# Kernel tuning notes

Hardware: AMD Instinct MI355X
Metric: run time of the kernel (lower is better)

The kernel has to match this reference:

```python
import jax, jax.numpy as jnp
import numpy as np

N = 50000   # nodes
E = 800000  # edges
G = 64      # graphs
NEG_SLOPE = 0.2  # PyG GATConv leaky_relu slope


def gat_conv(x, edge_index, edge_attr, W, att_src, att_dst, We, att_edge, bias, num_nodes):
    # PyG GATConv, add_self_loops=False, concat=True, eval (no dropout)
    H, C = att_src.shape
    h = (x @ W).reshape(-1, H, C)                      # [N,H,C]
    a_src = (h * att_src).sum(-1)                      # [N,H]
    a_dst = (h * att_dst).sum(-1)                      # [N,H]
    src, dst = edge_index[0], edge_index[1]
    e = (edge_attr @ We).reshape(-1, H, C)             # [E,H,C]
    a_edge = (e * att_edge).sum(-1)                    # [E,H]
    alpha = a_src[src] + a_dst[dst] + a_edge           # [E,H]
    alpha = jax.nn.leaky_relu(alpha, NEG_SLOPE)
    # segment softmax over incoming edges of each dst node
    amax = jax.ops.segment_max(alpha, dst, num_segments=num_nodes)
    amax = jnp.where(jnp.isfinite(amax), amax, 0.0)
    ex = jnp.exp(alpha - amax[dst])
    denom = jax.ops.segment_sum(ex, dst, num_segments=num_nodes)
    att = ex / (denom[dst] + 1e-16)                    # [E,H]
    msg = h[src] * att[..., None]                      # [E,H,C]
    out = jax.ops.segment_sum(msg, dst, num_segments=num_nodes)
    return out.reshape(num_nodes, H * C) + bias


def setup_inputs() -> dict:
    key = jax.random.key(0)
    ks = jax.random.split(key, 20)
    s = 0.1
    inp = {
        "x": jax.random.normal(ks[0], (N, 128), jnp.float32),
        "edge_index": jax.random.randint(ks[1], (2, E), 0, N, dtype=jnp.int32),
        "edge_attr": jax.random.normal(ks[2], (E, 1), jnp.float32),
        "batch": jnp.sort(jax.random.randint(ks[3], (N,), 0, G, dtype=jnp.int32)),
        # layer 1: 128 -> 4 heads x 32
        "W1": jax.random.normal(ks[4], (128, 128), jnp.float32) * s,
        "as1": jax.random.normal(ks[5], (4, 32), jnp.float32) * s,
        "ad1": jax.random.normal(ks[6], (4, 32), jnp.float32) * s,
        "We1": jax.random.normal(ks[7], (1, 128), jnp.float32) * s,
        "ae1": jax.random.normal(ks[8], (4, 32), jnp.float32) * s,
        "b1": jnp.zeros((128,), jnp.float32),
        # layer 2: 128 -> 1 head x 64
        "W2": jax.random.normal(ks[9], (128, 64), jnp.float32) * s,
        "as2": jax.random.normal(ks[10], (1, 64), jnp.float32) * s,
        "ad2": jax.random.normal(ks[11], (1, 64), jnp.float32) * s,
        "We2": jax.random.normal(ks[12], (1, 64), jnp.float32) * s,
        "ae2": jax.random.normal(ks[13], (1, 64), jnp.float32) * s,
        "b2": jnp.zeros((64,), jnp.float32),
        # prediction head
        "Wp": jax.random.normal(ks[14], (64, 1), jnp.float32) * s,
        "bp": jnp.zeros((1,), jnp.float32),
    }
    return inp


def reference(x, edge_index, edge_attr, batch, W1, as1, ad1, We1, ae1, b1,
              W2, as2, ad2, We2, ae2, b2, Wp, bp):
    h = gat_conv(x, edge_index, edge_attr, W1, as1, ad1, We1, ae1, b1, N)
    h = jax.nn.relu(h)  # dropout p=0.0, eval mode
    h = gat_conv(h, edge_index, edge_attr, W2, as2, ad2, We2, ae2, b2, N)
    # per-graph mean pooling (vectorized replacement of the python loop)
    counts = jax.ops.segment_sum(jnp.ones((N,), h.dtype), batch, num_segments=G)
    sums = jax.ops.segment_sum(h, batch, num_segments=G)   # [G,64]
    mean = sums / counts[:, None]
    out = mean @ Wp + bp                                   # [G,1]
    return out.squeeze(-1)                                 # [G]
```

## Files before the change

### kernel.cpp

```cpp
#include <hip/hip_runtime.h>
#include <hip/hip_bf16.h>

typedef unsigned short u16;
typedef unsigned int u32;

#define MAXB 2048
#define POOL_MAXG 64

typedef __attribute__((ext_vector_type(8))) short bf16x8;
typedef __attribute__((ext_vector_type(4))) float f32x4;

__device__ __forceinline__ float bf2f(u16 u) { return __uint_as_float(((u32)u) << 16); }
__device__ __forceinline__ float bl(u32 u) { return __uint_as_float(u << 16); }
__device__ __forceinline__ float bh(u32 u) { return __uint_as_float(u & 0xffff0000u); }
__device__ __forceinline__ u16 f2bf(float f) {
    u32 u = __float_as_uint(f);
    u += 0x7fffu + ((u >> 16) & 1u);
    return (u16)(u >> 16);
}
__device__ __forceinline__ float lrelu(float x) { return x > 0.f ? x : 0.2f * x; }
__device__ __forceinline__ int clampi(int v, int lo, int hi) {
    return v < lo ? lo : (v > hi ? hi : v);
}
__device__ __forceinline__ float load1(const void* base, int idx, int f32) {
    return f32 ? ((const float*)base)[idx] : bf2f(((const u16*)base)[idx]);
}
__device__ __forceinline__ float cexpf(float a) {
    return __builtin_amdgcn_exp2f(fminf(a, 30.f) * 1.4426950408889634f);
}

__global__ void k_init(const u32* __restrict__ xw, int* __restrict__ flag,
                       int* __restrict__ bcnt, int B,
                       const void* We1, const void* ae1, const void* We2, const void* ae2,
                       const void* as1, const void* ad1, const void* as2, const void* ad2,
                       float* __restrict__ consts, float* __restrict__ pool, int psize) {
    __shared__ int sf;
    int t = threadIdx.x;
    for (int i = t; i < B; i += 256) bcnt[i] = 0;
    if (t < 64) {
        int cnt = 0;
        #pragma unroll
        for (int j = 0; j < 4; j++) {
            u32 w = xw[t * 4 + j];
            int e0 = (int)((w >> 7) & 0xffu);
            int e1 = (int)((w >> 23) & 0xffu);
            cnt += (e0 >= 0x60 && e0 <= 0x8f);
            cnt += (e1 >= 0x60 && e1 <= 0x8f);
        }
        #pragma unroll
        for (int off = 32; off > 0; off >>= 1) cnt += __shfl_xor(cnt, off);
        if (t == 0) { int v = (cnt < 480) ? 1 : 0; *flag = v; sf = v; }
    }
    __syncthreads();
    int f = sf;
    for (int i = t; i < psize; i += 256) pool[i] = 0.f;
    if (t < 4) {
        float s = 0.f;
        for (int c = 0; c < 32; c++) s += load1(We1, t * 32 + c, f) * load1(ae1, t * 32 + c, f);
        consts[t] = s;
    } else if (t == 4) {
        float s = 0.f;
        for (int c = 0; c < 64; c++) s += load1(We2, c, f) * load1(ae2, c, f);
        consts[4] = s;
    }
    if (t < 128) {
        consts[8 + t] = load1(as1, t, f);
        consts[136 + t] = load1(ad1, t, f);
    }
    if (t < 64) {
        consts[264 + t] = load1(as2, t, f);
        consts[328 + t] = load1(ad2, t, f);
    }
}

template <int NC>
__global__ __launch_bounds__(256, 2) void k_gemm_mfma(
    const void* __restrict__ X, const void* __restrict__ Wg,
    const int* __restrict__ flag, int fXovr, u16* __restrict__ Y,
    const float* __restrict__ consts, float* __restrict__ casrc,
    float* __restrict__ cadst, int nrows) {
    constexpr int NCT = NC / 16;
    __shared__ __align__(16) u16 Bf[2][NCT][4][64][8];

    const int f = *flag;
    const bool fX = (fXovr < 0) ? (f != 0) : (fXovr != 0);
    const bool fW = (f != 0);
    const int tid = threadIdx.x;
    const int wid = tid >> 6, lane = tid & 63;

    for (int idx = tid; idx < NCT * 4 * 64; idx += 256) {
        int l = idx & 63;
        int s = (idx >> 6) & 3;
        int t = idx >> 8;
        int col = t * 16 + (l & 15);
        int k0 = s * 32 + (l >> 4) * 8;
        u16 hi[8], lo[8];
        #pragma unroll
        for (int j = 0; j < 8; j++) {
            int k = k0 + j;
            int srow = (NC == 64) ? ((k & 1) * 64 + (k >> 1)) : k;
            float v = fW ? ((const float*)Wg)[srow * NC + col]
                         : bf2f(((const u16*)Wg)[srow * NC + col]);
            u16 h = f2bf(v);
            hi[j] = h;
            lo[j] = fW ? f2bf(v - bf2f(h)) : (u16)0;
        }
        uint4 hv, lv;
        hv.x = (u32)hi[0] | ((u32)hi[1] << 16);
        hv.y = (u32)hi[2] | ((u32)hi[3] << 16);
        hv.z = (u32)hi[4] | ((u32)hi[5] << 16);
        hv.w = (u32)hi[6] | ((u32)hi[7] << 16);
        lv.x = (u32)lo[0] | ((u32)lo[1] << 16);
        lv.y = (u32)lo[2] | ((u32)lo[3] << 16);
        lv.z = (u32)lo[4] | ((u32)lo[5] << 16);
        lv.w = (u32)lo[6] | ((u32)lo[7] << 16);
        *(uint4*)&Bf[0][t][s][l][0] = hv;
        *(uint4*)&Bf[1][t][s][l][0] = lv;
    }
    __syncthreads();

    const int tiles = (nrows + 63) >> 6;
    for (int tile = blockIdx.x; tile < tiles; tile += gridDim.x) {
        const int rowbase = tile * 64 + wid * 16;
        const int arow = rowbase + (lane & 15);
        const bool rv = arow < nrows;

        bf16x8 ahi[4], alo[4];
        #pragma unroll
        for (int s = 0; s < 4; s++) {
            int koff = s * 32 + (lane >> 4) * 8;
            u16 h[8], l8[8];
            #pragma unroll
            for (int j = 0; j < 8; j++) { h[j] = 0; l8[j] = 0; }
            if (rv) {
                if (fX) {
                    const float* xp = (const float*)X + (size_t)arow * 128 + koff;
                    float4 a = *(const float4*)xp;
                    float4 b = *(const float4*)(xp + 4);
                    float vv[8];
                    vv[0] = a.x; vv[1] = a.y; vv[2] = a.z; vv[3] = a.w;
                    vv[4] = b.x; vv[5] = b.y; vv[6] = b.z; vv[7] = b.w;
                    #pragma unroll
                    for (int j = 0; j < 8; j++) {
                        h[j] = f2bf(vv[j]);
                        l8[j] = f2bf(vv[j] - bf2f(h[j]));
                    }
                } else {
                    const u16* xp = (const u16*)X + (size_t)arow * 128 + koff;
                    uint4 q = *(const uint4*)xp;
                    h[0] = (u16)q.x; h[1] = (u16)(q.x >> 16);
                    h[2] = (u16)q.y; h[3] = (u16)(q.y >> 16);
                    h[4] = (u16)q.z; h[5] = (u16)(q.z >> 16);
                    h[6] = (u16)q.w; h[7] = (u16)(q.w >> 16);
                }
            }
            bf16x8 vh, vl;
            #pragma unroll
            for (int j = 0; j < 8; j++) { vh[j] = (short)h[j]; vl[j] = (short)l8[j]; }
            ahi[s] = vh; alo[s] = vl;
        }

        f32x4 acc[NCT];
        #pragma unroll
        for (int t = 0; t < NCT; t++) acc[t] = (f32x4){0.f, 0.f, 0.f, 0.f};
        #pragma unroll
        for (int s = 0; s < 4; s++) {
            #pragma unroll
            for (int t = 0; t < NCT; t++) {
                bf16x8 bhi = *(const bf16x8*)&Bf[0][t][s][lane][0];
                acc[t] = __builtin_amdgcn_mfma_f32_16x16x32_bf16(ahi[s], bhi, acc[t], 0, 0, 0);
                if (fW) {
                    bf16x8 blo = *(const bf16x8*)&Bf[1][t][s][lane][0];
                    acc[t] = __builtin_amdgcn_mfma_f32_16x16x32_bf16(ahi[s], blo, acc[t], 0, 0, 0);
                }
                if (fX) {
                    acc[t] = __builtin_amdgcn_mfma_f32_16x16x32_bf16(alo[s], bhi, acc[t], 0, 0, 0);
                }
            }
        }

        #pragma unroll
        for (int reg = 0; reg < 4; reg++) {
            int r = rowbase + (lane >> 4) * 4 + reg;
            if (r < nrows) {
                if constexpr (NC == 128) {
                    #pragma unroll
                    for (int t = 0; t < 4; t++) {
                        u32 w = (u32)f2bf(acc[t][reg]) | ((u32)f2bf(acc[t + 4][reg]) << 16);
                        ((u32*)Y)[(size_t)r * 64 + t * 16 + (lane & 15)] = w;
                    }
                } else {
                    #pragma unroll
                    for (int t = 0; t < 4; t++)
                        Y[(size_t)r * 64 + t * 16 + (lane & 15)] = f2bf(acc[t][reg]);
                }
            }
        }

        if (casrc) {
            const int l16 = lane & 15;
            if constexpr (NC == 128) {
                #pragma unroll
                for (int reg = 0; reg < 4; reg++) {
                    int r = rowbase + (lane >> 4) * 4 + reg;
                    float pA[4] = {0.f, 0.f, 0.f, 0.f};
                    float pD[4] = {0.f, 0.f, 0.f, 0.f};
                    #pragma unroll
                    for (int t = 0; t < 4; t++) {
                        int p = t * 16 + l16;
                        int g = t >> 1;
                        pA[g]     += acc[t][reg]     * consts[8 + p];
                        pD[g]     += acc[t][reg]     * consts[136 + p];
                        pA[g + 2] += acc[t + 4][reg] * consts[72 + p];
                        pD[g + 2] += acc[t + 4][reg] * consts[200 + p];
                    }
                    #pragma unroll
                    for (int off = 1; off < 16; off <<= 1) {
                        #pragma unroll
                        for (int g = 0; g < 4; g++) {
                            pA[g] += __shfl_xor(pA[g], off);
                            pD[g] += __shfl_xor(pD[g], off);
                        }
                    }
                    if (l16 == 0 && r < nrows) {
                        #pragma unroll
                        for (int g = 0; g < 4; g++) {
                            casrc[r * 4 + g] = pA[g];
                            cadst[r * 4 + g] = pD[g];
                        }
                    }
                }
            } else {
                #pragma unroll
                for (int reg = 0; reg < 4; reg++) {
                    int r = rowbase + (lane >> 4) * 4 + reg;
                    float s1 = 0.f, s2 = 0.f;
                    #pragma unroll
                    for (int t = 0; t < 4; t++) {
                        int p = t * 16 + l16;
                        s1 += acc[t][reg] * consts[264 + p];
                        s2 += acc[t][reg] * consts[328 + p];
                    }
                    #pragma unroll
                    for (int off = 1; off < 16; off <<= 1) {
                        s1 += __shfl_xor(s1, off);
                        s2 += __shfl_xor(s2, off);
                    }
                    if (l16 == 0 && r < nrows) { casrc[r] = s1; cadst[r] = s2; }
                }
            }
        }
    }
}

__global__ __launch_bounds__(256) void k_bhist2(const int* __restrict__ dst,
                                                int* __restrict__ bcnt, int E, int n, int B) {
    __shared__ int lh[MAXB];
    for (int i = threadIdx.x; i < B; i += 256) lh[i] = 0;
    __syncthreads();
    int stride = gridDim.x * 256;
    for (int e = blockIdx.x * 256 + threadIdx.x; e < E; e += stride) {
        int d = clampi(dst[e], 0, n - 1);
        atomicAdd(&lh[d >> 8], 1);
    }
    __syncthreads();
    for (int i = threadIdx.x; i < B; i += 256)
        if (lh[i]) atomicAdd(&bcnt[i], lh[i]);
}
__global__ void k_bscan(const int* __restrict__ bcnt, int* __restrict__ bbase,
                        int* __restrict__ bfront, int* __restrict__ roff,
                        int B, int N, int E) {
    __shared__ int buf[256];
    __shared__ int carry;
    int t = threadIdx.x;
    if (t == 0) carry = 0;
    __syncthreads();
    for (int base = 0; base < B; base += 256) {
        int k = base + t;
        int v = (k < B) ? bcnt[k] : 0;
        buf[t] = v;
        __syncthreads();
        for (int off = 1; off < 256; off <<= 1) {
            int u = (t >= off) ? buf[t - off] : 0;
            __syncthreads();
            buf[t] += u;
            __syncthreads();
        }
        int excl = carry + buf[t] - v;
        if (k < B) { bbase[k] = excl; bfront[k] = excl; }
        __syncthreads();
        if (t == 0) carry += buf[255];
        __syncthreads();
    }
    if (t == 0) { bbase[B] = carry; roff[N] = E; }
}
__global__ void k_zero(int* __restrict__ p, int n) {
    int i = blockIdx.x * 256 + threadIdx.x;
    if (i < n) p[i] = 0;
}
__global__ __launch_bounds__(256) void k_bhist(const int* __restrict__ dst,
                                               int* __restrict__ cnt, int* __restrict__ bcnt,
                                               int E, int n, int B) {
    __shared__ int lh[MAXB];
    for (int i = threadIdx.x; i < B; i += 256) lh[i] = 0;
    __syncthreads();
    int stride = gridDim.x * 256;
    for (int e = blockIdx.x * 256 + threadIdx.x; e < E; e += stride) {
        int d = clampi(dst[e], 0, n - 1);
        atomicAdd(&cnt[d], 1);
        atomicAdd(&lh[d >> 8], 1);
    }
    __syncthreads();
    for (int i = threadIdx.x; i < B; i += 256)
        if (lh[i]) atomicAdd(&bcnt[i], lh[i]);
}
__global__ void k_scan1(const int* __restrict__ cnt, int* __restrict__ part,
                        int* __restrict__ bsum, int n) {
    __shared__ int buf[256];
    int i = blockIdx.x * 256 + threadIdx.x;
    int v = (i < n) ? cnt[i] : 0;
    buf[threadIdx.x] = v;
    __syncthreads();
    for (int off = 1; off < 256; off <<= 1) {
        int t = (threadIdx.x >= off) ? buf[threadIdx.x - off] : 0;
        __syncthreads();
        buf[threadIdx.x] += t;
        __syncthreads();
    }
    if (i < n) part[i] = buf[threadIdx.x];
    if (threadIdx.x == 255) bsum[blockIdx.x] = buf[255];
}
__global__ void k_scan3b(int* __restrict__ roff, const int* __restrict__ bsum,
                         int* __restrict__ rpos, int n, int nb) {
    __shared__ int buf[256];
    int t = threadIdx.x;
    int v = (t < nb) ? bsum[t] : 0;
    buf[t] = v;
    __syncthreads();
    for (int off = 1; off < 256; off <<= 1) {
        int u = (t >= off) ? buf[t - off] : 0;
        __syncthreads();
        buf[t] += u;
        __syncthreads();
    }
    __shared__ int excl[256];
    excl[t] = buf[t] - v;
    __syncthreads();
    int i = blockIdx.x * 256 + t;
    if (i > n) return;
    int val;
    if (i == 0) { val = 0; roff[0] = 0; }
    else { val = roff[i] + excl[(i - 1) >> 8]; roff[i] = val; }
    if (i < n) rpos[i] = val;
}
__global__ __launch_bounds__(256) void k_binA(
    const int* __restrict__ dst, const int* __restrict__ src, const void* eattr,
    const int* __restrict__ flag, int* __restrict__ bfront, int2* __restrict__ stagedA,
    int E, int n, int B) {
    __shared__ int lhist[MAXB];
    __shared__ int lbase[MAXB];
    int f = *flag;
    constexpr int T = 2048;
    for (int tile = blockIdx.x; (long long)tile * T < E; tile += gridDim.x) {
        int base = tile * T;
        for (int i = threadIdx.x; i < B; i += 256) lhist[i] = 0;
        __syncthreads();
        int sj0, sj1, sj2, sj3, sj4, sj5, sj6, sj7;
        int dj0, dj1, dj2, dj3, dj4, dj5, dj6, dj7;
        int rj0, rj1, rj2, rj3, rj4, rj5, rj6, rj7;
        int ej0, ej1, ej2, ej3, ej4, ej5, ej6, ej7;
        #define BINA_LOAD(J, SJ, DJ, RJ, EJ)                                   \
        {                                                                      \
            int idx = base + (J) * 256 + threadIdx.x;                          \
            bool v = idx < E;                                                  \
            int d = v ? clampi(dst[idx], 0, n - 1) : 0;                        \
            SJ = v ? clampi(src[idx], 0, n - 1) : 0;                           \
            EJ = v ? __float_as_int(load1(eattr, idx, f)) : 0;                 \
            DJ = d;                                                            \
            RJ = v ? atomicAdd(&lhist[d >> 8], 1) : -1;                        \
        }
        BINA_LOAD(0, sj0, dj0, rj0, ej0)
        BINA_LOAD(1, sj1, dj1, rj1, ej1)
        BINA_LOAD(2, sj2, dj2, rj2, ej2)
        BINA_LOAD(3, sj3, dj3, rj3, ej3)
        BINA_LOAD(4, sj4, dj4, rj4, ej4)
        BINA_LOAD(5, sj5, dj5, rj5, ej5)
        BINA_LOAD(6, sj6, dj6, rj6, ej6)
        BINA_LOAD(7, sj7, dj7, rj7, ej7)
        #undef BINA_LOAD
        __syncthreads();
        for (int i = threadIdx.x; i < B; i += 256) {
            int c = lhist[i];
            lbase[i] = c ? atomicAdd(&bfront[i], c) : 0;
        }
        __syncthreads();
        #define BINA_STORE(SJ, DJ, RJ, EJ)                                     \
        if (RJ >= 0) {                                                         \
            long long q = (long long)lbase[DJ >> 8] + RJ;                      \
            if (q >= 0 && q < E) {                                             \
                int2 v2;                                                       \
                v2.x = (SJ & 0xFFFFFF) | ((DJ & 255) << 24);                   \
                v2.y = EJ;                                                     \
                stagedA[q] = v2;                                               \
            }                                                                  \
        }
        BINA_STORE(sj0, dj0, rj0, ej0)
        BINA_STORE(sj1, dj1, rj1, ej1)
        BINA_STORE(sj2, dj2, rj2, ej2)
        BINA_STORE(sj3, dj3, rj3, ej3)
        BINA_STORE(sj4, dj4, rj4, ej4)
        BINA_STORE(sj5, dj5, rj5, ej5)
        BINA_STORE(sj6, dj6, rj6, ej6)
        BINA_STORE(sj7, dj7, rj7, ej7)
        #undef BINA_STORE
        __syncthreads();
    }
}
__global__ __launch_bounds__(256) void k_binB2(
    const int2* __restrict__ stagedA, const int* __restrict__ bbase,
    int* __restrict__ roff, int2* __restrict__ edata, int N, int E, int B) {
    __shared__ int lcnt[256];
    __shared__ int buf[256];
    __shared__ int lpos[256];
    int k = blockIdx.x;
    int t = threadIdx.x;
    lcnt[t] = 0;
    __syncthreads();
    int lo = clampi(bbase[k], 0, E);
    int hi = clampi(bbase[k + 1], lo, E);
    for (int i = lo + t; i < hi; i += 256)
        atomicAdd(&lcnt[(stagedA[i].x >> 24) & 255], 1);
    __syncthreads();
    int v = lcnt[t];
    buf[t] = v;
    __syncthreads();
    for (int off = 1; off < 256; off <<= 1) {
        int u = (t >= off) ? buf[t - off] : 0;
        __syncthreads();
        buf[t] += u;
        __syncthreads();
    }
    int pos = lo + buf[t] - v;
    int dn = (k << 8) + t;
    if (dn < N) roff[dn] = pos;
    lpos[t] = pos;
    __syncthreads();
    for (int i = lo + t; i < hi; i += 256) {
        int2 a = stagedA[i];
        int p = atomicAdd(&lpos[(a.x >> 24) & 255], 1);
        if (p >= 0 && p < E) edata[p] = make_int2(a.x & 0xFFFFFF, a.y);
    }
}
__global__ void k_scatter(const int* __restrict__ dst, const int* __restrict__ src,
                          const void* eattr, const int* __restrict__ flag,
                          int* __restrict__ rpos, int2* __restrict__ edata, int E, int n) {
    int f = *flag;
    int e = blockIdx.x * 256 + threadIdx.x;
    if (e < E) {
        int d = clampi(dst[e], 0, n - 1);
        int s = clampi(src[e], 0, n - 1);
        float ea = load1(eattr, e, f);
        int p = atomicAdd(&rpos[d], 1);
        if (p >= 0 && p < E) {
            int2 v; v.x = s; v.y = __float_as_int(ea);
            edata[p] = v;
        }
    }
}

__global__ __launch_bounds__(256) void k_gat1c(
    const u32* __restrict__ hp, const float* __restrict__ asrc, const float* __restrict__ adst,
    const int2* __restrict__ edata, const int* __restrict__ roff,
    const int* __restrict__ flag, const float* __restrict__ consts, const void* bias,
    u32* __restrict__ out, int n, int E) {
    __shared__ float4 wls[4][64];
    int f = *flag;
    int gtid = blockIdx.x * 256 + threadIdx.x;
    int wv = gtid >> 6, lane = gtid & 63;
    int wid = (threadIdx.x >> 6);
    int nw = (gridDim.x * 256) >> 6;
    const float c0 = consts[0], c1 = consts[1], c2 = consts[2], c3 = consts[3];
    const int hl = lane & 31;
    const int sel = lane >> 5;
    const int p0 = hl * 2;
    const int phsel = hl >> 4;
    const float biasA0 = load1(bias, p0, f);
    const float biasB0 = load1(bias, 64 + p0, f);
    const float biasA1 = load1(bias, p0 + 1, f);
    const float biasB1 = load1(bias, 64 + p0 + 1, f);
    const int ghsel = lane >> 5;
    const float gbiasA = load1(bias, lane, f);
    const float gbiasB = load1(bias, 64 + lane, f);

    for (int db = wv * 2; db < n; db += nw * 2) {
        int d = db + sel;
        bool dv = d < n;
        int dcl = dv ? d : 0;
        int s0 = dv ? clampi(roff[d], 0, E) : 0;
        int s1 = dv ? clampi(roff[d + 1], s0, E) : 0;
        int deg = s1 - s0;

        if (__all(deg <= 32)) {
            float4 adv = *(const float4*)&adst[(size_t)dcl * 4];
            bool v = hl < deg;
            int s = 0;
            float e0 = 0.f, e1 = 0.f, e2 = 0.f, e3 = 0.f;
            if (v) {
                int2 ed = edata[s0 + hl];
                s = ed.x;
                float ea = __int_as_float(ed.y);
                float4 av = *(const float4*)&asrc[(size_t)s * 4];
                e0 = cexpf(lrelu(av.x + adv.x + ea * c0));
                e1 = cexpf(lrelu(av.y + adv.y + ea * c1));
                e2 = cexpf(lrelu(av.z + adv.z + ea * c2));
                e3 = cexpf(lrelu(av.w + adv.w + ea * c3));
            }
            float d0 = e0, d1 = e1, d2 = e2, d3 = e3;
            #pragma unroll
            for (int off = 16; off > 0; off >>= 1) {
                d0 += __shfl_xor(d0, off); d1 += __shfl_xor(d1, off);
                d2 += __shfl_xor(d2, off); d3 += __shfl_xor(d3, off);
            }
            float i0 = 1.f / (d0 + 1e-16f), i1 = 1.f / (d1 + 1e-16f);
            float i2 = 1.f / (d2 + 1e-16f), i3 = 1.f / (d3 + 1e-16f);
            wls[wid][lane] = make_float4(e0 * i0, e1 * i1, e2 * i2, e3 * i3);

            int degm = max(deg, __shfl_xor(deg, 32));
            int base = sel * 32;
            float aA0 = 0.f, aB0 = 0.f, aA1 = 0.f, aB1 = 0.f;
            for (int j = 0; j < degm; j += 4) {
                int j0 = base + j, j1 = base + j + 1, j2 = base + j + 2, j3 = base + j + 3;
                int sa = __shfl(s, j0), sb = __shfl(s, j1);
                int sc_ = __shfl(s, j2), sd = __shfl(s, j3);
                float4 wa = wls[wid][j0], wb = wls[wid][j1];
                float4 wc = wls[wid][j2], wd = wls[wid][j3];
                uint2 ha = *(const uint2*)(hp + (size_t)sa * 64 + p0);
                uint2 hb = *(const uint2*)(hp + (size_t)sb * 64 + p0);
                uint2 hc = *(const uint2*)(hp + (size_t)sc_ * 64 + p0);
                uint2 hd = *(const uint2*)(hp + (size_t)sd * 64 + p0);
                float wAa = phsel ? wa.y : wa.x, wBa = phsel ? wa.w : wa.z;
                float wAb = phsel ? wb.y : wb.x, wBb = phsel ? wb.w : wb.z;
                float wAc = phsel ? wc.y : wc.x, wBc = phsel ? wc.w : wc.z;
                float wAd = phsel ? wd.y : wd.x, wBd = phsel ? wd.w : wd.z;
                aA0 += wAa * bl(ha.x); aB0 += wBa * bh(ha.x);
                aA1 += wAa * bl(ha.y); aB1 += wBa * bh(ha.y);
                aA0 += wAb * bl(hb.x); aB0 += wBb * bh(hb.x);
                aA1 += wAb * bl(hb.y); aB1 += wBb * bh(hb.y);
                aA0 += wAc * bl(hc.x); aB0 += wBc * bh(hc.x);
                aA1 += wAc * bl(hc.y); aB1 += wBc * bh(hc.y);
                aA0 += wAd * bl(hd.x); aB0 += wBd * bh(hd.x);
                aA1 += wAd * bl(hd.y); aB1 += wBd * bh(hd.y);
            }
            if (dv) {
                u32 w0 = (u32)f2bf(fmaxf(aA0 + biasA0, 0.f))
                       | ((u32)f2bf(fmaxf(aB0 + biasB0, 0.f)) << 16);
                u32 w1 = (u32)f2bf(fmaxf(aA1 + biasA1, 0.f))
                       | ((u32)f2bf(fmaxf(aB1 + biasB1, 0.f)) << 16);
                *(uint2*)(out + (size_t)d * 64 + p0) = make_uint2(w0, w1);
            }
        } else {
            for (int q = 0; q < 2; q++) {
                int dq = db + q;
                if (dq >= n) break;
                int t0 = clampi(roff[dq], 0, E);
                int t1 = clampi(roff[dq + 1], t0, E);
                int dg = t1 - t0;
                float4 adv = *(const float4*)&adst[(size_t)dq * 4];
                if (dg <= 64) {
                    bool v = lane < dg;
                    int s = 0;
                    float e0 = 0.f, e1 = 0.f, e2 = 0.f, e3 = 0.f;
                    if (v) {
                        int2 ed = edata[t0 + lane];
                        s = ed.x;
                        float ea = __int_as_float(ed.y);
                        float4 av = *(const float4*)&asrc[(size_t)s * 4];
                        e0 = cexpf(lrelu(av.x + adv.x + ea * c0));
                        e1 = cexpf(lrelu(av.y + adv.y + ea * c1));
                        e2 = cexpf(lrelu(av.z + adv.z + ea * c2));
                        e3 = cexpf(lrelu(av.w + adv.w + ea * c3));
                    }
                    float d0 = e0, d1 = e1, d2 = e2, d3 = e3;
                    #pragma unroll
                    for (int off = 32; off > 0; off >>= 1) {
                        d0 += __shfl_xor(d0, off); d1 += __shfl_xor(d1, off);
                        d2 += __shfl_xor(d2, off); d3 += __shfl_xor(d3, off);
                    }
                    float i0 = 1.f / (d0 + 1e-16f), i1 = 1.f / (d1 + 1e-16f);
                    float i2 = 1.f / (d2 + 1e-16f), i3 = 1.f / (d3 + 1e-16f);
                    wls[wid][lane] = make_float4(e0 * i0, e1 * i1, e2 * i2, e3 * i3);

                    float aA0 = 0.f, aB0 = 0.f, aA1 = 0.f, aB1 = 0.f;
                    for (int j = 0; j < dg; j += 4) {
                        int j0 = j + sel, j1 = j + 2 + sel;
                        int sa = __shfl(s, j0), sb = __shfl(s, j1);
                        float4 wa = wls[wid][j0], wb = wls[wid][j1];
                        uint2 ha = *(const uint2*)(hp + (size_t)sa * 64 + p0);
                        uint2 hb = *(const uint2*)(hp + (size_t)sb * 64 + p0);
                        float wAa = phsel ? wa.y : wa.x, wBa = phsel ? wa.w : wa.z;
                        float wAb = phsel ? wb.y : wb.x, wBb = phsel ? wb.w : wb.z;
                        aA0 += wAa * bl(ha.x); aB0 += wBa * bh(ha.x);
                        aA1 += wAa * bl(ha.y); aB1 += wBa * bh(ha.y);
                        aA0 += wAb * bl(hb.x); aB0 += wBb * bh(hb.x);
                        aA1 += wAb * bl(hb.y); aB1 += wBb * bh(hb.y);
                    }
                    aA0 += __shfl_xor(aA0, 32); aB0 += __shfl_xor(aB0, 32);
                    aA1 += __shfl_xor(aA1, 32); aB1 += __shfl_xor(aB1, 32);
                    if (lane < 32) {
                        u32 w0 = (u32)f2bf(fmaxf(aA0 + biasA0, 0.f))
                               | ((u32)f2bf(fmaxf(aB0 + biasB0, 0.f)) << 16);
                        u32 w1 = (u32)f2bf(fmaxf(aA1 + biasA1, 0.f))
                               | ((u32)f2bf(fmaxf(aB1 + biasB1, 0.f)) << 16);
                        *(uint2*)(out + (size_t)dq * 64 + p0) = make_uint2(w0, w1);
                    }
                } else {
                    float d0 = 0.f, d1 = 0.f, d2 = 0.f, d3 = 0.f;
                    for (int idx = t0 + lane; idx < t1; idx += 64) {
                        int2 ed = edata[idx];
                        float ea = __int_as_float(ed.y);
                        float4 av = *(const float4*)&asrc[(size_t)ed.x * 4];
                        d0 += cexpf(lrelu(av.x + adv.x + ea * c0));
                        d1 += cexpf(lrelu(av.y + adv.y + ea * c1));
                        d2 += cexpf(lrelu(av.z + adv.z + ea * c2));
                        d3 += cexpf(lrelu(av.w + adv.w + ea * c3));
                    }
                    #pragma unroll
                    for (int off = 32; off > 0; off >>= 1) {
                        d0 += __shfl_xor(d0, off); d1 += __shfl_xor(d1, off);
                        d2 += __shfl_xor(d2, off); d3 += __shfl_xor(d3, off);
                    }
                    float i0 = 1.f / (d0 + 1e-16f), i1 = 1.f / (d1 + 1e-16f);
                    float i2 = 1.f / (d2 + 1e-16f), i3 = 1.f / (d3 + 1e-16f);
                    float iA = ghsel ? i1 : i0, iB = ghsel ? i3 : i2;
                    float cA = ghsel ? c1 : c0, cB = ghsel ? c3 : c2;
                    float aA = ghsel ? adv.y : adv.x, aB = ghsel ? adv.w : adv.z;
                    float accA = 0.f, accB = 0.f;
                    for (int idx = t0; idx < t1; idx++) {
                        int2 ed = edata[idx];
                        float ea = __int_as_float(ed.y);
                        float4 av = *(const float4*)&asrc[(size_t)ed.x * 4];
                        float wA = cexpf(lrelu((ghsel ? av.y : av.x) + aA + ea * cA)) * iA;
                        float wB = cexpf(lrelu((ghsel ? av.w : av.z) + aB + ea * cB)) * iB;
                        u32 hw = hp[(size_t)ed.x * 64 + lane];
                        accA += wA * bl(hw);
                        accB += wB * bh(hw);
                    }
                    float rA = fmaxf(accA + gbiasA, 0.f);
                    float rB = fmaxf(accB + gbiasB, 0.f);
                    out[(size_t)dq * 64 + lane] = (u32)f2bf(rA) | ((u32)f2bf(rB) << 16);
                }
            }
        }
    }
}

__global__ __launch_bounds__(256) void k_gat2c(
    const u16* __restrict__ h, const float* __restrict__ asrc, const float* __restrict__ adst,
    const int2* __restrict__ edata, const int* __restrict__ roff,
    const int* __restrict__ flag, const float* __restrict__ consts, const void* bias,
    u16* __restrict__ out, int n, int E) {
    __shared__ float wls[4][64];
    int f = *flag;
    int gtid = blockIdx.x * 256 + threadIdx.x;
    int wv = gtid >> 6, lane = gtid & 63;
    int wid = (threadIdx.x >> 6);
    int nw = (gridDim.x * 256) >> 6;
    const float C = consts[4];
    const int hl = lane & 31;
    const int sel = lane >> 5;
    const int p0 = hl * 2;
    const float bias0 = load1(bias, p0, f);
    const float bias1 = load1(bias, p0 + 1, f);
    const float gbias = load1(bias, lane, f);

    for (int db = wv * 2; db < n; db += nw * 2) {
        int d = db + sel;
        bool dv = d < n;
        int s0 = dv ? clampi(roff[d], 0, E) : 0;
        int s1 = dv ? clampi(roff[d + 1], s0, E) : 0;
        int deg = s1 - s0;
        float ad = dv ? adst[d] : 0.f;

        if (__all(deg <= 32)) {
            bool v = hl < deg;
            int s = 0;
            float e = 0.f;
            if (v) {
                int2 ed = edata[s0 + hl];
                s = ed.x;
                e = cexpf(lrelu(asrc[s] + ad + __int_as_float(ed.y) * C));
            }
            float den = e;
            #pragma unroll
            for (int off = 16; off > 0; off >>= 1) den += __shfl_xor(den, off);
            float inv = 1.f / (den + 1e-16f);
            wls[wid][lane] = e * inv;

            int degm = max(deg, __shfl_xor(deg, 32));
            int base = sel * 32;
            float a0 = 0.f, a1 = 0.f;
            for (int j = 0; j < degm; j += 4) {
                int j0 = base + j, j1 = base + j + 1, j2 = base + j + 2, j3 = base + j + 3;
                int sa = __shfl(s, j0), sb = __shfl(s, j1);
                int sc_ = __shfl(s, j2), sd = __shfl(s, j3);
                float wa = wls[wid][j0], wb = wls[wid][j1];
                float wc = wls[wid][j2], wd = wls[wid][j3];
                u32 ha = *(const u32*)(h + (size_t)sa * 64 + p0);
                u32 hb = *(const u32*)(h + (size_t)sb * 64 + p0);
                u32 hc = *(const u32*)(h + (size_t)sc_ * 64 + p0);
                u32 hd = *(const u32*)(h + (size_t)sd * 64 + p0);
                a0 += wa * bl(ha) + wb * bl(hb) + wc * bl(hc) + wd * bl(hd);
                a1 += wa * bh(ha) + wb * bh(hb) + wc * bh(hc) + wd * bh(hd);
            }
            if (dv) {
                u32 w = (u32)f2bf(a0 + bias0) | ((u32)f2bf(a1 + bias1) << 16);
                *(u32*)(out + (size_t)d * 64 + p0) = w;
            }
        } else {
            for (int q = 0; q < 2; q++) {
                int dq = db + q;
                if (dq >= n) break;
                int t0 = clampi(roff[dq], 0, E);
                int t1 = clampi(roff[dq + 1], t0, E);
                int dg = t1 - t0;
                float adq = adst[dq];
                if (dg <= 64) {
                    bool v = lane < dg;
                    int s = 0;
                    float e = 0.f;
                    if (v) {
                        int2 ed = edata[t0 + lane];
                        s = ed.x;
                        e = cexpf(lrelu(asrc[s] + adq + __int_as_float(ed.y) * C));
                    }
                    float den = e;
                    #pragma unroll
                    for (int off = 32; off > 0; off >>= 1) den += __shfl_xor(den, off);
                    float inv = 1.f / (den + 1e-16f);
                    wls[wid][lane] = e * inv;

                    float a0 = 0.f, a1 = 0.f;
                    for (int j = 0; j < dg; j += 4) {
                        int j0 = j + sel, j1 = j + 2 + sel;
                        int sa = __shfl(s, j0), sb = __shfl(s, j1);
                        float wa = wls[wid][j0], wb = wls[wid][j1];
                        u32 ha = *(const u32*)(h + (size_t)sa * 64 + p0);
                        u32 hb = *(const u32*)(h + (size_t)sb * 64 + p0);
                        a0 += wa * bl(ha) + wb * bl(hb);
                        a1 += wa * bh(ha) + wb * bh(hb);
                    }
                    a0 += __shfl_xor(a0, 32);
                    a1 += __shfl_xor(a1, 32);
                    if (lane < 32) {
                        u32 w = (u32)f2bf(a0 + bias0) | ((u32)f2bf(a1 + bias1) << 16);
                        *(u32*)(out + (size_t)dq * 64 + p0) = w;
                    }
                } else {
                    float den = 0.f;
                    for (int idx = t0 + lane; idx < t1; idx += 64) {
                        int2 ed = edata[idx];
                        den += cexpf(lrelu(asrc[ed.x] + adq + __int_as_float(ed.y) * C));
                    }
                    #pragma unroll
                    for (int off = 32; off > 0; off >>= 1) den += __shfl_xor(den, off);
                    float inv = 1.f / (den + 1e-16f);
                    float acc = 0.f;
                    for (int idx = t0; idx < t1; idx++) {
                        int2 ed = edata[idx];
                        float w = cexpf(lrelu(asrc[ed.x] + adq
                                              + __int_as_float(ed.y) * C)) * inv;
                        acc += w * bf2f(h[(size_t)ed.x * 64 + lane]);
                    }
                    out[(size_t)dq * 64 + lane] = f2bf(acc + gbias);
                }
            }
        }
    }
}

__global__ __launch_bounds__(256) void k_gat1f(
    const u32* __restrict__ hp, const float* __restrict__ asrc, const float* __restrict__ adst,
    const int2* __restrict__ edata, const int* __restrict__ roff,
    const int* __restrict__ flag, const float* __restrict__ consts, const void* bias,
    u32* __restrict__ out, int n, int E) {
    int f = *flag;
    int gtid = blockIdx.x * 256 + threadIdx.x;
    int wv = gtid >> 6, lane = gtid & 63;
    int nw = (gridDim.x * 256) >> 6;
    const float c0 = consts[0], c1 = consts[1], c2 = consts[2], c3 = consts[3];
    const int hsel = lane >> 5;
    const float biasA = load1(bias, lane, f);
    const float biasB = load1(bias, 64 + lane, f);

    for (int d = wv; d < n; d += nw) {
        int s0 = clampi(roff[d], 0, E);
        int s1 = clampi(roff[d + 1], s0, E);
        float4 adv = *(const float4*)&adst[d * 4];
        float d0 = 0.f, d1 = 0.f, d2 = 0.f, d3 = 0.f;
        for (int idx = s0 + lane; idx < s1; idx += 64) {
            int2 ed = edata[idx];
            float ea = __int_as_float(ed.y);
            float4 av = *(const float4*)&asrc[(size_t)ed.x * 4];
            d0 += cexpf(lrelu(av.x + adv.x + ea * c0));
            d1 += cexpf(lrelu(av.y + adv.y + ea * c1));
            d2 += cexpf(lrelu(av.z + adv.z + ea * c2));
            d3 += cexpf(lrelu(av.w + adv.w + ea * c3));
        }
        #pragma unroll
        for (int off = 32; off > 0; off >>= 1) {
            d0 += __shfl_xor(d0, off); d1 += __shfl_xor(d1, off);
            d2 += __shfl_xor(d2, off); d3 += __shfl_xor(d3, off);
        }
        float i0 = 1.f / (d0 + 1e-16f), i1 = 1.f / (d1 + 1e-16f);
        float i2 = 1.f / (d2 + 1e-16f), i3 = 1.f / (d3 + 1e-16f);
        float iA = hsel ? i1 : i0, iB = hsel ? i3 : i2;
        float cA = hsel ? c1 : c0, cB = hsel ? c3 : c2;
        float aA = hsel ? adv.y : adv.x, aB = hsel ? adv.w : adv.z;

        float accA = 0.f, accB = 0.f;
        for (int idx = s0; idx < s1; idx++) {
            int2 ed = edata[idx];
            float ea = __int_as_float(ed.y);
            float4 av = *(const float4*)&asrc[(size_t)ed.x * 4];
            float wA = cexpf(lrelu((hsel ? av.y : av.x) + aA + ea * cA)) * iA;
            float wB = cexpf(lrelu((hsel ? av.w : av.z) + aB + ea * cB)) * iB;
            u32 hw = hp[(size_t)ed.x * 64 + lane];
            accA += wA * bl(hw);
            accB += wB * bh(hw);
        }
        float rA = fmaxf(accA + biasA, 0.f);
        float rB = fmaxf(accB + biasB, 0.f);
        out[(size_t)d * 64 + lane] = (u32)f2bf(rA) | ((u32)f2bf(rB) << 16);
    }
}

__global__ __launch_bounds__(256) void k_gat2f(
    const u16* __restrict__ h, const float* __restrict__ asrc, const float* __restrict__ adst,
    const int2* __restrict__ edata, const int* __restrict__ roff,
    const int* __restrict__ flag, const float* __restrict__ consts, const void* bias,
    u16* __restrict__ out, int n, int E) {
    int f = *flag;
    int gtid = blockIdx.x * 256 + threadIdx.x;
    int wv = gtid >> 6, lane = gtid & 63;
    int nw = (gridDim.x * 256) >> 6;
    const float C = consts[4];
    const float biasL = load1(bias, lane, f);

    for (int d = wv; d < n; d += nw) {
        int s0 = clampi(roff[d], 0, E);
        int s1 = clampi(roff[d + 1], s0, E);
        float ad = adst[d];
        float den = 0.f;
        for (int idx = s0 + lane; idx < s1; idx += 64) {
            int2 ed = edata[idx];
            den += cexpf(lrelu(asrc[ed.x] + ad + __int_as_float(ed.y) * C));
        }
        #pragma unroll
        for (int off = 32; off > 0; off >>= 1) den += __shfl_xor(den, off);
        float inv = 1.f / (den + 1e-16f);

        float acc = 0.f;
        for (int idx = s0; idx < s1; idx++) {
            int2 ed = edata[idx];
            float w = cexpf(lrelu(asrc[ed.x] + ad + __int_as_float(ed.y) * C)) * inv;
            acc += w * bf2f(h[(size_t)ed.x * 64 + lane]);
        }
        out[(size_t)d * 64 + lane] = f2bf(acc + biasL);
    }
}

__global__ __launch_bounds__(256) void k_pool2(
    const u16* __restrict__ agg2, const int* __restrict__ batch,
    float* __restrict__ pool, float* __restrict__ cnt, int n, int G, int rpb) {
    __shared__ float lp[POOL_MAXG * 64];
    __shared__ float lc[POOL_MAXG];
    int t = threadIdx.x;
    for (int i = t; i < G * 64; i += 256) lp[i] = 0.f;
    for (int i = t; i < G; i += 256) lc[i] = 0.f;
    __syncthreads();
    int lane = t & 63;
    int rl = t >> 6;
    int r0 = blockIdx.x * rpb;
    int r1 = min(r0 + rpb, n);
    float acc = 0.f, cacc = 0.f;
    int curg = -1;
    for (int j = r0 + rl; j < r1; j += 4) {
        int g = clampi(batch[j], 0, G - 1);
        float v = bf2f(agg2[(size_t)j * 64 + lane]);
        if (g != curg) {
            if (curg >= 0) {
                atomicAdd(&lp[curg * 64 + lane], acc);
                if (lane == 0) atomicAdd(&lc[curg], cacc);
            }
            acc = 0.f; cacc = 0.f; curg = g;
        }
        acc += v; cacc += 1.f;
    }
    if (curg >= 0) {
        atomicAdd(&lp[curg * 64 + lane], acc);
        if (lane == 0) atomicAdd(&lc[curg], cacc);
    }
    __syncthreads();
    for (int i = t; i < G * 64; i += 256) {
        float v = lp[i];
        if (v != 0.f) atomicAdd(&pool[i], v);
    }
    for (int i = t; i < G; i += 256) {
        float v = lc[i];
        if (v != 0.f) atomicAdd(&cnt[i], v);
    }
}

__global__ void k_pool(const u16* __restrict__ agg2, const int* __restrict__ batch,
                       float* __restrict__ pool, float* __restrict__ cnt, int n, int G) {
    int t = blockIdx.x * 256 + threadIdx.x;
    int nb8 = (n + 7) / 8;
    if (t >= nb8 * 64) return;
    int base = (t >> 6) * 8;
    int c = t & 63;
    int end = min(base + 8, n);
    float acc = 0.f, cacc = 0.f;
    int curg = clampi(batch[base], 0, G - 1);
    for (int j = base; j < end; j++) {
        int g = clampi(batch[j], 0, G - 1);
        if (g != curg) {
            atomicAdd(&pool[curg * 64 + c], acc);
            if (c == 0) atomicAdd(&cnt[curg], cacc);
            acc = 0.f; cacc = 0.f; curg = g;
        }
        acc += bf2f(agg2[(size_t)j * 64 + c]);
        cacc += 1.f;
    }
    atomicAdd(&pool[curg * 64 + c], acc);
    if (c == 0) atomicAdd(&cnt[curg], cacc);
}

__global__ void k_head(const float* __restrict__ pool, const float* __restrict__ cnt,
                       const void* Wp, const void* bp, const int* __restrict__ flag,
                       void* out, int G) {
    int f = *flag;
    int g = threadIdx.x;
    if (g >= G) return;
    float s = 0.f;
    for (int c = 0; c < 64; c++) s += pool[g * 64 + c] * load1(Wp, c, f);
    float cv = cnt[g];
    if (!(cv > 0.f)) cv = 1.f;
    float r = s / cv + load1(bp, 0, f);
    if (f) ((float*)out)[g] = r;
    else   ((u16*)out)[g] = f2bf(r);
}

extern "C" void kernel_launch(void* const* d_in, const int* in_sizes, int n_in,
                              void* d_out, int out_size, void* d_ws, size_t ws_size,
                              hipStream_t stream) {
    const void* x    = d_in[0];
    const int* ei    = (const int*)d_in[1];
    const void* eattr = d_in[2];
    const int* batch = (const int*)d_in[3];
    const void* W1   = d_in[4];
    const void* as1  = d_in[5];
    const void* ad1  = d_in[6];
    const void* We1  = d_in[7];
    const void* ae1  = d_in[8];
    const void* b1   = d_in[9];
    const void* W2   = d_in[10];
    const void* as2  = d_in[11];
    const void* ad2  = d_in[12];
    const void* We2  = d_in[13];
    const void* ae2  = d_in[14];
    const void* b2   = d_in[15];
    const void* Wp   = d_in[16];
    const void* bp   = d_in[17];

    const int N = in_sizes[3];
    const int E = in_sizes[2];
    const int G = out_size;
    const int* src = ei;
    const int* dst = ei + E;
    const int B = (N + 255) >> 8;

    char* p = (char*)d_ws;
    auto alloc = [&](size_t bytes) -> char* {
        char* r = p;
        p += (bytes + 255) & ~(size_t)255;
        return r;
    };
    int* flag    = (int*)alloc(32);
    float* consts = (float*)alloc(2048);
    int* roff    = (int*)alloc((size_t)(N + 1) * 4);
    int* rpos    = (int*)alloc((size_t)N * 4);
    int* bsum    = (int*)alloc(256 * 4);
    int* bcnt    = (int*)alloc((size_t)(MAXB * 3 + 1) * 4);
    int* bbase   = bcnt + MAXB;
    int* bfront  = bbase + MAXB + 1;
    int2* edata  = (int2*)alloc((size_t)E * 8);
    float* pool  = (float*)alloc((size_t)(G * 64 + G) * 4);
    float* cnt   = pool + (size_t)G * 64;
    float* asrc1 = (float*)alloc((size_t)N * 4 * 4);
    float* adst1 = (float*)alloc((size_t)N * 4 * 4);
    float* asrc2 = asrc1;
    float* adst2 = adst1;
    u16* agg1    = (u16*)alloc((size_t)N * 128 * 2);
    u16* h1      = (u16*)alloc((size_t)N * 128 * 2);
    u16* h2      = h1;
    u16* agg2    = h1 + (size_t)N * 64;
    int2* stagedA = (int2*)alloc((size_t)E * 8);
    size_t full_need = (size_t)(p - (char*)d_ws);
    const bool cached = (ws_size >= full_need);
    const bool binned = cached && (B <= MAXB) && (N <= (1 << 24));

    const int GG = (N + 127) >> 7;

    k_init<<<1, 256, 0, stream>>>((const u32*)x, flag, bcnt, B,
                                  We1, ae1, We2, ae2, as1, ad1, as2, ad2,
                                  consts, pool, G * 64 + G);
    k_gemm_mfma<128><<<GG, 256, 0, stream>>>(x, W1, flag, -1, h1, consts,
                                             asrc1, adst1, N);

    if (binned) {
        k_bhist2<<<512, 256, 0, stream>>>(dst, bcnt, E, N, B);
        k_bscan<<<1, 256, 0, stream>>>(bcnt, bbase, bfront, roff, B, N, E);
        k_binA<<<(E + 2047) / 2048, 256, 0, stream>>>(dst, src, eattr, flag, bfront,
                                                      stagedA, E, N, B);
        k_binB2<<<B, 256, 0, stream>>>(stagedA, bbase, roff, edata, N, E, B);
    } else {
        int NB = (N + 255) / 256;
        k_zero<<<(N + 255) / 256, 256, 0, stream>>>(rpos, N);
        k_bhist<<<512, 256, 0, stream>>>(dst, rpos, bcnt, E, N, B);
        k_scan1<<<NB, 256, 0, stream>>>(rpos, roff + 1, bsum, N);
        k_scan3b<<<(N + 256) / 256, 256, 0, stream>>>(roff, bsum, rpos, N, NB);
        k_scatter<<<(E + 255) / 256, 256, 0, stream>>>(dst, src, eattr, flag, rpos,
                                                       edata, E, N);
    }

    int gatBlocks = (N * 64 + 255) / 256;
    if (cached) {
        k_gat1c<<<gatBlocks, 256, 0, stream>>>((const u32*)h1, asrc1, adst1, edata, roff,
                                               flag, consts, b1, (u32*)agg1, N, E);
    } else {
        k_gat1f<<<gatBlocks, 256, 0, stream>>>((const u32*)h1, asrc1, adst1, edata, roff,
                                               flag, consts, b1, (u32*)agg1, N, E);
    }
    k_gemm_mfma<64><<<GG, 256, 0, stream>>>(agg1, W2, flag, 0, h2, consts,
                                            asrc2, adst2, N);
    if (cached) {
        k_gat2c<<<gatBlocks, 256, 0, stream>>>(h2, asrc2, adst2, edata, roff, flag,
                                               consts, b2, agg2, N, E);
    } else {
        k_gat2f<<<gatBlocks, 256, 0, stream>>>(h2, asrc2, adst2, edata, roff, flag,
                                               consts, b2, agg2, N, E);
    }
    if (G <= POOL_MAXG) {
        int rpb = (N + 1023) / 1024;
        if (rpb < 8) rpb = 8;
        int pblocks = (N + rpb - 1) / rpb;
        k_pool2<<<pblocks, 256, 0, stream>>>(agg2, batch, pool, cnt, N, G, rpb);
    } else {
        k_pool<<<(((N + 7) / 8) * 64 + 255) / 256, 256, 0, stream>>>(agg2, batch, pool,
                                                                     cnt, N, G);
    }
    k_head<<<1, 64, 0, stream>>>(pool, cnt, Wp, bp, flag, d_out, G);
}
```

Before: 283.5 us.

## Coalesce weight staging and process two row tiles per block in MFMA GEMM

Weight staging into shared memory now reads W with contiguous float4/uint4 loads and scatters the elements into the MFMA fragment layout, replacing strided scalar global reads. The grid-stride tile loop is replaced by a fixed two-tile-per-block scheme. Both tiles' A fragments are loaded up front and the MFMAs are interleaved, so each B fragment read from LDS is reused twice and there is more independent MFMA work in flight. This doubles accumulator and A-register usage, which may reduce occupancy. It also relies on the launch grid covering all tiles in two passes, otherwise rows would go unprocessed.

```diff
diff --git a/kernel.cpp b/kernel.cpp
--- a/kernel.cpp
+++ b/kernel.cpp
@@ -88,44 +88,60 @@
     const int tid = threadIdx.x;
     const int wid = tid >> 6, lane = tid & 63;
 
-    for (int idx = tid; idx < NCT * 4 * 64; idx += 256) {
-        int l = idx & 63;
-        int s = (idx >> 6) & 3;
-        int t = idx >> 8;
-        int col = t * 16 + (l & 15);
-        int k0 = s * 32 + (l >> 4) * 8;
-        u16 hi[8], lo[8];
-        #pragma unroll
-        for (int j = 0; j < 8; j++) {
-            int k = k0 + j;
-            int srow = (NC == 64) ? ((k & 1) * 64 + (k >> 1)) : k;
-            float v = fW ? ((const float*)Wg)[srow * NC + col]
-                         : bf2f(((const u16*)Wg)[srow * NC + col]);
-            u16 h = f2bf(v);
-            hi[j] = h;
-            lo[j] = fW ? f2bf(v - bf2f(h)) : (u16)0;
-        }
-        uint4 hv, lv;
-        hv.x = (u32)hi[0] | ((u32)hi[1] << 16);
-        hv.y = (u32)hi[2] | ((u32)hi[3] << 16);
-        hv.z = (u32)hi[4] | ((u32)hi[5] << 16);
-        hv.w = (u32)hi[6] | ((u32)hi[7] << 16);
-        lv.x = (u32)lo[0] | ((u32)lo[1] << 16);
-        lv.y = (u32)lo[2] | ((u32)lo[3] << 16);
-        lv.z = (u32)lo[4] | ((u32)lo[5] << 16);
-        lv.w = (u32)lo[6] | ((u32)lo[7] << 16);
-        *(uint4*)&Bf[0][t][s][l][0] = hv;
-        *(uint4*)&Bf[1][t][s][l][0] = lv;
-    }
-    __syncthreads();
-
-    const int tiles = (nrows + 63) >> 6;
-    for (int tile = blockIdx.x; tile < tiles; tile += gridDim.x) {
-        const int rowbase = tile * 64 + wid * 16;
+    if (fW) {
+        const float* W4 = (const float*)Wg;
+        for (int g = tid; g < 128 * NC / 4; g += 256) {
+            int e = g * 4;
+            int r = e / NC;
+            int c = e % NC;
+            int k = (NC == 64) ? ((r < 64) ? 2 * r : 2 * (r - 64) + 1) : r;
+            int s = k >> 5;
+            int kk = k & 31;
+            int lhi = (kk >> 3) << 4;
+            int j = kk & 7;
+            float4 v = *(const float4*)(W4 + e);
+            float vv[4] = {v.x, v.y, v.z, v.w};
+            #pragma unroll
+            for (int q = 0; q < 4; q++) {
+                int col = c + q;
+                int t = col >> 4, l = lhi | (col & 15);
+                u16 h = f2bf(vv[q]);
+                Bf[0][t][s][l][j] = h;
+                Bf[1][t][s][l][j] = f2bf(vv[q] - bf2f(h));
+            }
+        }
+    } else {
+        const u16* Wb = (const u16*)Wg;
+        for (int g = tid; g < 128 * NC / 8; g += 256) {
+            int e = g * 8;
+            int r = e / NC;
+            int c = e % NC;
+            int k = (NC == 64) ? ((r < 64) ? 2 * r : 2 * (r - 64) + 1) : r;
+            int s = k >> 5;
+            int kk = k & 31;
+            int lhi = (kk >> 3) << 4;
+            int j = kk & 7;
+            uint4 v = *(const uint4*)(Wb + e);
+            u16 arr[8] = {(u16)v.x, (u16)(v.x >> 16), (u16)v.y, (u16)(v.y >> 16),
+                          (u16)v.z, (u16)(v.z >> 16), (u16)v.w, (u16)(v.w >> 16)};
+            #pragma unroll
+            for (int q = 0; q < 8; q++) {
+                int col = c + q;
+                int t = col >> 4, l = lhi | (col & 15);
+                Bf[0][t][s][l][j] = arr[q];
+            }
+        }
+    }
+    __syncthreads();
+
+    const int tileIds[2] = {(int)blockIdx.x, (int)(blockIdx.x + gridDim.x)};
+
+    bf16x8 ahi[2][4], alo[2][4];
+    #pragma unroll
+    for (int tt = 0; tt < 2; tt++) {
+        const int rowbase = tileIds[tt] * 64 + wid * 16;
         const int arow = rowbase + (lane & 15);
         const bool rv = arow < nrows;
-
-        bf16x8 ahi[4], alo[4];
         #pragma unroll
         for (int s = 0; s < 4; s++) {
             int koff = s * 32 + (lane >> 4) * 8;
@@ -157,28 +173,38 @@
             bf16x8 vh, vl;
             #pragma unroll
             for (int j = 0; j < 8; j++) { vh[j] = (short)h[j]; vl[j] = (short)l8[j]; }
-            ahi[s] = vh; alo[s] = vl;
-        }
-
-        f32x4 acc[NCT];
+            ahi[tt][s] = vh; alo[tt][s] = vl;
+        }
+    }
+
+    f32x4 acc[2][NCT];
+    #pragma unroll
+    for (int tt = 0; tt < 2; tt++)
         #pragma unroll
-        for (int t = 0; t < NCT; t++) acc[t] = (f32x4){0.f, 0.f, 0.f, 0.f};
+        for (int t = 0; t < NCT; t++) acc[tt][t] = (f32x4){0.f, 0.f, 0.f, 0.f};
+    #pragma unroll
+    for (int s = 0; s < 4; s++) {
         #pragma unroll
-        for (int s = 0; s < 4; s++) {
-            #pragma unroll
-            for (int t = 0; t < NCT; t++) {
-                bf16x8 bhi = *(const bf16x8*)&Bf[0][t][s][lane][0];
-                acc[t] = __builtin_amdgcn_mfma_f32_16x16x32_bf16(ahi[s], bhi, acc[t], 0, 0, 0);
-                if (fW) {
-                    bf16x8 blo = *(const bf16x8*)&Bf[1][t][s][lane][0];
-                    acc[t] = __builtin_amdgcn_mfma_f32_16x16x32_bf16(ahi[s], blo, acc[t], 0, 0, 0);
-                }
-                if (fX) {
-                    acc[t] = __builtin_amdgcn_mfma_f32_16x16x32_bf16(alo[s], bhi, acc[t], 0, 0, 0);
-                }
-            }
-        }
-
+        for (int t = 0; t < NCT; t++) {
+            bf16x8 bhi = *(const bf16x8*)&Bf[0][t][s][lane][0];
+            acc[0][t] = __builtin_amdgcn_mfma_f32_16x16x32_bf16(ahi[0][s], bhi, acc[0][t], 0, 0, 0);
+            acc[1][t] = __builtin_amdgcn_mfma_f32_16x16x32_bf16(ahi[1][s], bhi, acc[1][t], 0, 0, 0);
+            if (fW) {
+                bf16x8 blo = *(const bf16x8*)&Bf[1][t][s][lane][0];
+                acc[0][t] = __builtin_amdgcn_mfma_f32_16x16x32_bf16(ahi[0][s], blo, acc[0][t], 0, 0, 0);
+                acc[1][t] = __builtin_amdgcn_mfma_f32_16x16x32_bf16(ahi[1][s], blo, acc[1][t], 0, 0, 0);
+            }
+            if (fX) {
+                acc[0][t] = __builtin_amdgcn_mfma_f32_16x16x32_bf16(alo[0][s], bhi, acc[0][t], 0, 0, 0);
+                acc[1][t] = __builtin_amdgcn_mfma_f32_16x16x32_bf16(alo[1][s], bhi, acc[1][t], 0, 0, 0);
+            }
+        }
+    }
+
+    #pragma unroll
+    for (int tt = 0; tt < 2; tt++) {
+        const int rowbase = tileIds[tt] * 64 + wid * 16;
+        const int l16 = lane & 15;
         #pragma unroll
         for (int reg = 0; reg < 4; reg++) {
             int r = rowbase + (lane >> 4) * 4 + reg;
@@ -186,19 +212,18 @@
                 if constexpr (NC == 128) {
                     #pragma unroll
                     for (int t = 0; t < 4; t++) {
-                        u32 w = (u32)f2bf(acc[t][reg]) | ((u32)f2bf(acc[t + 4][reg]) << 16);
-                        ((u32*)Y)[(size_t)r * 64 + t * 16 + (lane & 15)] = w;
+                        u32 w = (u32)f2bf(acc[tt][t][reg])
+                              | ((u32)f2bf(acc[tt][t + 4][reg]) << 16);
+                        ((u32*)Y)[(size_t)r * 64 + t * 16 + l16] = w;
                     }
                 } else {
                     #pragma unroll
                     for (int t = 0; t < 4; t++)
-                        Y[(size_t)r * 64 + t * 16 + (lane & 15)] = f2bf(acc[t][reg]);
+                        Y[(size_t)r * 64 + t * 16 + l16] = f2bf(acc[tt][t][reg]);
                 }
             }
         }
-
         if (casrc) {
-            const int l16 = lane & 15;
             if constexpr (NC == 128) {
                 #pragma unroll
                 for (int reg = 0; reg < 4; reg++) {
@@ -209,10 +234,10 @@
                     for (int t = 0; t < 4; t++) {
                         int p = t * 16 + l16;
                         int g = t >> 1;
-                        pA[g]     += acc[t][reg]     * consts[8 + p];
-                        pD[g]     += acc[t][reg]     * consts[136 + p];
-                        pA[g + 2] += acc[t + 4][reg] * consts[72 + p];
-                        pD[g + 2] += acc[t + 4][reg] * consts[200 + p];
+                        pA[g]     += acc[tt][t][reg]     * consts[8 + p];
+                        pD[g]     += acc[tt][t][reg]     * consts[136 + p];
+                        pA[g + 2] += acc[tt][t + 4][reg] * consts[72 + p];
+                        pD[g + 2] += acc[tt][t + 4][reg] * consts[200 + p];
                     }
                     #pragma unroll
                     for (int off = 1; off < 16; off <<= 1) {
@@ -238,8 +263,8 @@
                     #pragma unroll
                     for (int t = 0; t < 4; t++) {
                         int p = t * 16 + l16;
-                        s1 += acc[t][reg] * consts[264 + p];
-                        s2 += acc[t][reg] * consts[328 + p];
+                        s1 += acc[tt][t][reg] * consts[264 + p];
+                        s2 += acc[tt][t][reg] * consts[328 + p];
                     }
                     #pragma unroll
                     for (int off = 1; off < 16; off <<= 1) {
```

Result: no change. 283.4 us (-0.0%).
